# Kernel tuning notes

Measured on AMD Instinct MI355X. Metric: run time of the kernel, lower is better.

Reference implementation:

```python
import jax, jax.numpy as jnp
import numpy as np
from jax.scipy.special import logsumexp

SIGMA = 1.0
EPSILON = 1.0
MAX_ITER = 10


def _gaussian_kernel(x, y, sigma):
    # x: (b, l, d), y: (b, k, d) -> (b, l, k) negative-kernel matrix exp(-||x-y||^2 / (2 sigma^2))
    outer = jnp.einsum('bld,bkd->blk', x, y)
    norm_x = jnp.sum(x * x, axis=2)
    norm_y = jnp.sum(y * y, axis=2)
    dist = (norm_x[:, :, None] + norm_y[:, None, :] - 2.0 * outer) / (2.0 * sigma ** 2)
    return jnp.exp(-jnp.maximum(dist, 0.0))


def setup_inputs() -> dict:
    key = jax.random.key(0)
    kx, ka, ky, kb = jax.random.split(key, 4)
    B, L, K, D = 8, 2048, 2048, 32
    return {
        'x': jax.random.normal(kx, (B, L, D), dtype=jnp.float32),
        'a': jax.random.normal(ka, (B, L), dtype=jnp.float32),
        'y': jax.random.normal(ky, (B, K, D), dtype=jnp.float32),
        'b': jax.random.normal(kb, (B, K), dtype=jnp.float32),
    }


def _sinkhorn_potentials(x, a, y, b):
    sg = jax.lax.stop_gradient
    # Kernel matrices (carry gradient wrt x, y); weights a, b are detached inside kernels.
    Kxx = _gaussian_kernel(x, x, SIGMA) / EPSILON + sg(a)[:, None, :]
    Kyx_base = _gaussian_kernel(y, x, SIGMA)
    Kyx = Kyx_base / EPSILON + sg(a)[:, None, :]
    Kxy = jnp.swapaxes(Kyx_base, 1, 2) / EPSILON + sg(b)[:, None, :]
    Kyy = _gaussian_kernel(y, y, SIGMA) / EPSILON + sg(b)[:, None, :]

    # Sinkhorn loop runs under no_grad in the original: stop-gradient kernels.
    Kxx_s, Kyx_s, Kxy_s, Kyy_s = sg(Kxx), sg(Kyx), sg(Kxy), sg(Kyy)

    def step(carry, _):
        fxx, fyx, fxy, fyy = carry
        # sequential (Gauss-Seidel) update order matches the torch dict order xx, yx, xy, yy
        fxx = 0.5 * fxx - 0.5 * logsumexp(Kxx_s + fxx[:, None, :], axis=2)
        fyx = 0.5 * fyx - 0.5 * logsumexp(Kyx_s + fxy[:, None, :], axis=2)  # uses old fxy
        fxy = 0.5 * fxy - 0.5 * logsumexp(Kxy_s + fyx[:, None, :], axis=2)  # uses new fyx
        fyy = 0.5 * fyy - 0.5 * logsumexp(Kyy_s + fyy[:, None, :], axis=2)
        return (fxx, fyx, fxy, fyy), None

    init = (jnp.zeros_like(a), jnp.zeros_like(b), jnp.zeros_like(a), jnp.zeros_like(b))
    (fxx, fyx, fxy, fyy), _ = jax.lax.scan(step, init, None, length=MAX_ITER)

    # Final differentiable extrapolation step (potentials are detached constants).
    fe_xx = -logsumexp(Kxx + fxx[:, None, :], axis=2)
    fe_yx = -logsumexp(Kyx + fxy[:, None, :], axis=2)
    fe_xy = -logsumexp(Kxy + fyx[:, None, :], axis=2)
    fe_yy = -logsumexp(Kyy + fyy[:, None, :], axis=2)
    f = fe_xy - fe_xx  # (b, l)
    g = fe_yx - fe_yy  # (b, k)
    return f, g


def reference(x, a, y, b):
    f, g = _sinkhorn_potentials(x, a, y, b)
    res = jnp.sum(f * jnp.exp(a), axis=1) + jnp.sum(g * jnp.exp(b), axis=1)
    return res * EPSILON  # (batch,)
```

## Files before the change

kernel.cpp:

```cpp
#include <hip/hip_runtime.h>
#include <hip/hip_bf16.h>

#define B_ 8
#define N_ 2048
#define D_ 32
#define CAP 4096
#define EM1_DIAG 1.7182818284590452f

typedef __attribute__((ext_vector_type(8))) short short8;
typedef __attribute__((ext_vector_type(4))) float f32x4;

__global__ void setup_kernel(const float* __restrict__ x, const float* __restrict__ y,
                             unsigned short* __restrict__ xb, unsigned short* __restrict__ yb,
                             float* __restrict__ NX, float* __restrict__ NY,
                             int* __restrict__ cnt)
{
    int t = blockIdx.x * 256 + threadIdx.x;
    const float* src = (t < 16384) ? x : y;
    unsigned short* dstb = (t < 16384) ? xb : yb;
    float* dstn = (t < 16384) ? NX : NY;
    int row = (t < 16384) ? t : (t - 16384);
    const float* p = src + (size_t)row * D_;
    float ss = 0.f;
    unsigned short tmp[D_];
    #pragma unroll
    for (int k = 0; k < D_; k++) {
        float v = p[k];
        ss = fmaf(v, v, ss);
        __hip_bfloat16 h = __float2bfloat16(v);
        tmp[k] = *reinterpret_cast<unsigned short*>(&h);
    }
    #pragma unroll
    for (int k = 0; k < D_; k++) dstb[(size_t)row * D_ + k] = tmp[k];
    dstn[row] = ss * 0.5f;
    if (t < 24) cnt[t] = 0;
}

__global__ __launch_bounds__(256) void discover_kernel(
    const unsigned short* __restrict__ xb, const unsigned short* __restrict__ yb,
    const float* __restrict__ NX, const float* __restrict__ NY,
    int* __restrict__ cnt, uint2* __restrict__ lists)
{
    int m = blockIdx.x >> 8;
    int rem = blockIdx.x & 255;
    int batch = rem >> 5;
    int rowblk = rem & 31;
    const unsigned short* rd = (m == 0) ? xb : yb;
    const float*          rN = (m == 0) ? NX : NY;
    const unsigned short* cd = (m == 1) ? yb : xb;
    const float*          cN = (m == 1) ? NY : NX;

    const int tid = threadIdx.x, lane = tid & 63, wv = tid >> 6;
    const int r0 = rowblk * 64;
    const size_t rowbase = (size_t)batch * N_ + r0;

    short8 afrag[4];
    f32x4 cinit[4];
    #pragma unroll
    for (int g = 0; g < 4; g++) {
        afrag[g] = *reinterpret_cast<const short8*>(
            rd + (rowbase + g * 16 + (lane & 15)) * D_ + (lane >> 4) * 8);
        #pragma unroll
        for (int r = 0; r < 4; r++)
            cinit[g][r] = -rN[rowbase + g * 16 + (lane >> 4) * 4 + r];
    }
    const unsigned short* cdB = cd + (size_t)batch * N_ * D_;
    const float* cNB = cN + batch * N_;
    const int slot = m * 8 + batch;
    uint2* L = lists + (size_t)slot * CAP;

    #pragma unroll 4
    for (int cc = 0; cc < 32; ++cc) {
        int col = wv * 512 + cc * 16 + (lane & 15);
        short8 bfrag = *reinterpret_cast<const short8*>(
            cdB + (size_t)col * D_ + (lane >> 4) * 8);
        float ny = cNB[col];
        f32x4 d[4];
        #pragma unroll
        for (int g = 0; g < 4; g++)
            d[g] = __builtin_amdgcn_mfma_f32_16x16x32_bf16(afrag[g], bfrag, cinit[g], 0, 0, 0);
        float mx = d[0][0];
        #pragma unroll
        for (int g = 0; g < 4; g++)
            #pragma unroll
            for (int r = 0; r < 4; r++) mx = fmaxf(mx, d[g][r]);
        if (__any(mx > ny - 10.0f)) {
            #pragma unroll
            for (int g = 0; g < 4; g++) {
                #pragma unroll
                for (int r = 0; r < 4; r++) {
                    float dist = ny - d[g][r];
                    if (dist < 10.0f) {
                        int i = r0 + g * 16 + (lane >> 4) * 4 + r;
                        if (m == 2 || i != col) {
                            float Gv = __expf(-fmaxf(dist, 0.f));
                            float em1 = __expf(Gv) - 1.0f;
                            int idx = atomicAdd(&cnt[slot], 1);
                            if (idx < CAP)
                                L[idx] = make_uint2(((unsigned)i << 16) | (unsigned)col,
                                                    __float_as_uint(em1));
                        }
                    }
                }
            }
        }
    }
}

__global__ __launch_bounds__(1024) void sinkhorn_kernel(
    const float* __restrict__ a_in, const float* __restrict__ b_in,
    const int* __restrict__ cnt, const uint2* __restrict__ lists,
    float* __restrict__ out)
{
    __shared__ float f[4][N_];
    __shared__ float wsh[2][N_];
    __shared__ float ev[N_];
    __shared__ float acc[N_];
    __shared__ float red[16], red2[16];
    __shared__ float resacc;

    const int batch = blockIdx.x;
    const int t = threadIdx.x, lane = t & 63, wv = t >> 6;

    #pragma unroll
    for (int q = 0; q < 2; q++) {
        int j = t + 1024 * q;
        wsh[0][j] = a_in[batch * N_ + j];
        wsh[1][j] = b_in[batch * N_ + j];
        f[0][j] = 0.f; f[1][j] = 0.f; f[2][j] = 0.f; f[3][j] = 0.f;
    }
    if (t == 0) resacc = 0.f;

    const int nxx = min(cnt[0 * 8 + batch], CAP);
    const int nyy = min(cnt[1 * 8 + batch], CAP);
    const int nyx = min(cnt[2 * 8 + batch], CAP);
    const uint2* Lxx = lists + (size_t)(0 * 8 + batch) * CAP;
    const uint2* Lyy = lists + (size_t)(1 * 8 + batch) * CAP;
    const uint2* Lyx = lists + (size_t)(2 * 8 + batch) * CAP;
    __syncthreads();

    auto pass = [&](const float* wc, const float* cfv, float* fd,
                    const uint2* L, int n, bool tr, bool diag,
                    bool fin, const float* rw, float sgn) {
        float c0 = wc[t] + cfv[t];
        float c1 = wc[t + 1024] + cfv[t + 1024];
        float mloc = fmaxf(c0, c1);
        #pragma unroll
        for (int off = 1; off < 64; off <<= 1)
            mloc = fmaxf(mloc, __shfl_xor(mloc, off, 64));
        if (lane == 0) red[wv] = mloc;
        __syncthreads();
        float M = red[0];
        #pragma unroll
        for (int k = 1; k < 16; k++) M = fmaxf(M, red[k]);
        float e0 = __expf(c0 - M), e1 = __expf(c1 - M);
        ev[t] = e0; ev[t + 1024] = e1;
        acc[t]        = diag ? e0 * EM1_DIAG : 0.f;
        acc[t + 1024] = diag ? e1 * EM1_DIAG : 0.f;
        float ss = e0 + e1;
        #pragma unroll
        for (int off = 1; off < 64; off <<= 1)
            ss += __shfl_xor(ss, off, 64);
        if (lane == 0) red2[wv] = ss;
        __syncthreads();
        float S0 = red2[0];
        #pragma unroll
        for (int k = 1; k < 16; k++) S0 += red2[k];
        for (int p = t; p < n; p += 1024) {
            uint2 ent = L[p];
            int i = tr ? (int)(ent.x & 0xFFFFu) : (int)(ent.x >> 16);
            int j = tr ? (int)(ent.x >> 16)     : (int)(ent.x & 0xFFFFu);
            atomicAdd(&acc[i], ev[j] * __uint_as_float(ent.y));
        }
        __syncthreads();
        float r0v = M + __logf(S0 + acc[t]);
        float r1v = M + __logf(S0 + acc[t + 1024]);
        if (!fin) {
            fd[t]        = 0.5f * fd[t]        - 0.5f * r0v;
            fd[t + 1024] = 0.5f * fd[t + 1024] - 0.5f * r1v;
        } else {
            float ctr = sgn * (-r0v) * __expf(rw[t])
                      + sgn * (-r1v) * __expf(rw[t + 1024]);
            #pragma unroll
            for (int off = 1; off < 64; off <<= 1)
                ctr += __shfl_xor(ctr, off, 64);
            if (lane == 0) atomicAdd(&resacc, ctr);
        }
        __syncthreads();
    };

    for (int it = 0; it < 10; ++it) {
        pass(wsh[0], f[0], f[0], Lxx, nxx, false, true,  false, nullptr, 0.f);
        pass(wsh[0], f[2], f[1], Lyx, nyx, false, false, false, nullptr, 0.f);
        pass(wsh[1], f[1], f[2], Lyx, nyx, true,  false, false, nullptr, 0.f);
        pass(wsh[1], f[3], f[3], Lyy, nyy, false, true,  false, nullptr, 0.f);
    }
    pass(wsh[0], f[0], nullptr, Lxx, nxx, false, true,  true, wsh[0], -1.f);
    pass(wsh[0], f[2], nullptr, Lyx, nyx, false, false, true, wsh[1], +1.f);
    pass(wsh[1], f[1], nullptr, Lyx, nyx, true,  false, true, wsh[0], +1.f);
    pass(wsh[1], f[3], nullptr, Lyy, nyy, false, true,  true, wsh[1], -1.f);

    if (t == 0) out[batch] = resacc;
}

extern "C" void kernel_launch(void* const* d_in, const int* in_sizes, int n_in,
                              void* d_out, int out_size, void* d_ws, size_t ws_size,
                              hipStream_t stream)
{
    const float* x = (const float*)d_in[0];
    const float* a = (const float*)d_in[1];
    const float* y = (const float*)d_in[2];
    const float* b = (const float*)d_in[3];
    float* out = (float*)d_out;

    char* ws = (char*)d_ws;
    size_t o = 0;
    unsigned short* xb = (unsigned short*)(ws + o); o += (size_t)B_ * N_ * D_ * 2;
    unsigned short* yb = (unsigned short*)(ws + o); o += (size_t)B_ * N_ * D_ * 2;
    float* NX = (float*)(ws + o); o += (size_t)B_ * N_ * 4;
    float* NY = (float*)(ws + o); o += (size_t)B_ * N_ * 4;
    int* cnt = (int*)(ws + o); o += 128;
    uint2* lists = (uint2*)(ws + o); o += (size_t)3 * 8 * CAP * 8;

    setup_kernel<<<128, 256, 0, stream>>>(x, y, xb, yb, NX, NY, cnt);
    discover_kernel<<<3 * 256, 256, 0, stream>>>(xb, yb, NX, NY, cnt, lists);
    sinkhorn_kernel<<<B_, 1024, 0, stream>>>(a, b, cnt, lists, out);
}
```

Measured before the change: 205.9 us.

## Merge independent Sinkhorn passes per stage and use a fixed logsumexp shift

The xx, yx and yy potential updates do not depend on each other, so they now run together in one stage. The dependent xy update runs in a second stage, which removes about half of the block-wide barriers per iteration. The per-pass max reduction is replaced by a constant shift (M=8) with exp(a-8) and exp(b-8) computed once up front, and the first 2048 sparse-list entries are held in registers across iterations. The fixed shift assumes that weights and potentials stay within float exp range, which trades numerical robustness on extreme inputs for fewer reductions.

```diff
diff --git a/kernel.cpp b/kernel.cpp
--- a/kernel.cpp
+++ b/kernel.cpp
@@ -6,6 +6,8 @@
 #define D_ 32
 #define CAP 4096
 #define EM1_DIAG 1.7182818284590452f
+#define M_   8.0f
+#define EM_  2980.9579870417283f
 
 typedef __attribute__((ext_vector_type(8))) short short8;
 typedef __attribute__((ext_vector_type(4))) float f32x4;
@@ -113,23 +115,14 @@
     float* __restrict__ out)
 {
     __shared__ float f[4][N_];
-    __shared__ float wsh[2][N_];
-    __shared__ float ev[N_];
-    __shared__ float acc[N_];
-    __shared__ float red[16], red2[16];
+    __shared__ float ew[2][N_];
+    __shared__ float ev[4][N_];
+    __shared__ float acc[4][N_];
+    __shared__ float red2[4][16];
     __shared__ float resacc;
 
     const int batch = blockIdx.x;
     const int t = threadIdx.x, lane = t & 63, wv = t >> 6;
-
-    #pragma unroll
-    for (int q = 0; q < 2; q++) {
-        int j = t + 1024 * q;
-        wsh[0][j] = a_in[batch * N_ + j];
-        wsh[1][j] = b_in[batch * N_ + j];
-        f[0][j] = 0.f; f[1][j] = 0.f; f[2][j] = 0.f; f[3][j] = 0.f;
-    }
-    if (t == 0) resacc = 0.f;
 
     const int nxx = min(cnt[0 * 8 + batch], CAP);
     const int nyy = min(cnt[1 * 8 + batch], CAP);
@@ -137,70 +130,149 @@
     const uint2* Lxx = lists + (size_t)(0 * 8 + batch) * CAP;
     const uint2* Lyy = lists + (size_t)(1 * 8 + batch) * CAP;
     const uint2* Lyx = lists + (size_t)(2 * 8 + batch) * CAP;
+
+    uint2 rxx[2], ryy[2], ryx[2];
+    #pragma unroll
+    for (int q = 0; q < 2; q++) {
+        int p = t + 1024 * q;
+        rxx[q] = (p < nxx) ? Lxx[p] : make_uint2(0u, 0u);
+        ryy[q] = (p < nyy) ? Lyy[p] : make_uint2(0u, 0u);
+        ryx[q] = (p < nyx) ? Lyx[p] : make_uint2(0u, 0u);
+    }
+
+    #pragma unroll
+    for (int q = 0; q < 2; q++) {
+        int j = t + 1024 * q;
+        ew[0][j] = __expf(a_in[batch * N_ + j] - M_);
+        ew[1][j] = __expf(b_in[batch * N_ + j] - M_);
+        f[0][j] = 0.f; f[1][j] = 0.f; f[2][j] = 0.f; f[3][j] = 0.f;
+    }
+    if (t == 0) resacc = 0.f;
     __syncthreads();
 
-    auto pass = [&](const float* wc, const float* cfv, float* fd,
-                    const uint2* L, int n, bool tr, bool diag,
-                    bool fin, const float* rw, float sgn) {
-        float c0 = wc[t] + cfv[t];
-        float c1 = wc[t + 1024] + cfv[t + 1024];
-        float mloc = fmaxf(c0, c1);
-        #pragma unroll
-        for (int off = 1; off < 64; off <<= 1)
-            mloc = fmaxf(mloc, __shfl_xor(mloc, off, 64));
-        if (lane == 0) red[wv] = mloc;
-        __syncthreads();
-        float M = red[0];
-        #pragma unroll
-        for (int k = 1; k < 16; k++) M = fmaxf(M, red[k]);
-        float e0 = __expf(c0 - M), e1 = __expf(c1 - M);
-        ev[t] = e0; ev[t + 1024] = e1;
-        acc[t]        = diag ? e0 * EM1_DIAG : 0.f;
-        acc[t + 1024] = diag ? e1 * EM1_DIAG : 0.f;
-        float ss = e0 + e1;
-        #pragma unroll
-        for (int off = 1; off < 64; off <<= 1)
-            ss += __shfl_xor(ss, off, 64);
-        if (lane == 0) red2[wv] = ss;
-        __syncthreads();
-        float S0 = red2[0];
-        #pragma unroll
-        for (int k = 1; k < 16; k++) S0 += red2[k];
-        for (int p = t; p < n; p += 1024) {
-            uint2 ent = L[p];
-            int i = tr ? (int)(ent.x & 0xFFFFu) : (int)(ent.x >> 16);
-            int j = tr ? (int)(ent.x >> 16)     : (int)(ent.x & 0xFFFFu);
-            atomicAdd(&acc[i], ev[j] * __uint_as_float(ent.y));
-        }
-        __syncthreads();
-        float r0v = M + __logf(S0 + acc[t]);
-        float r1v = M + __logf(S0 + acc[t + 1024]);
-        if (!fin) {
-            fd[t]        = 0.5f * fd[t]        - 0.5f * r0v;
-            fd[t + 1024] = 0.5f * fd[t + 1024] - 0.5f * r1v;
-        } else {
-            float ctr = sgn * (-r0v) * __expf(rw[t])
-                      + sgn * (-r1v) * __expf(rw[t + 1024]);
-            #pragma unroll
-            for (int off = 1; off < 64; off <<= 1)
-                ctr += __shfl_xor(ctr, off, 64);
-            if (lane == 0) atomicAdd(&resacc, ctr);
+    auto stageA = [&]() {
+        float ss0 = 0.f, ss1 = 0.f, ss2 = 0.f;
+        #pragma unroll
+        for (int q = 0; q < 2; q++) {
+            int j = t + 1024 * q;
+            float e0 = ew[0][j] * __expf(f[0][j]); ev[0][j] = e0; acc[0][j] = e0 * EM1_DIAG; ss0 += e0;
+            float e1 = ew[0][j] * __expf(f[2][j]); ev[1][j] = e1; acc[1][j] = 0.f;           ss1 += e1;
+            float e2 = ew[1][j] * __expf(f[3][j]); ev[2][j] = e2; acc[2][j] = e2 * EM1_DIAG; ss2 += e2;
+        }
+        #pragma unroll
+        for (int off = 1; off < 64; off <<= 1) {
+            ss0 += __shfl_xor(ss0, off, 64);
+            ss1 += __shfl_xor(ss1, off, 64);
+            ss2 += __shfl_xor(ss2, off, 64);
+        }
+        if (lane == 0) { red2[0][wv] = ss0; red2[1][wv] = ss1; red2[2][wv] = ss2; }
+        __syncthreads();
+        float S0 = red2[0][0], S1 = red2[1][0], S2 = red2[2][0];
+        #pragma unroll
+        for (int k = 1; k < 16; k++) { S0 += red2[0][k]; S1 += red2[1][k]; S2 += red2[2][k]; }
+        #pragma unroll
+        for (int q = 0; q < 2; q++) {
+            int p = t + 1024 * q;
+            if (p < nxx) { uint2 e = rxx[q]; atomicAdd(&acc[0][e.x >> 16], ev[0][e.x & 0xFFFFu] * __uint_as_float(e.y)); }
+            if (p < nyx) { uint2 e = ryx[q]; atomicAdd(&acc[1][e.x >> 16], ev[1][e.x & 0xFFFFu] * __uint_as_float(e.y)); }
+            if (p < nyy) { uint2 e = ryy[q]; atomicAdd(&acc[2][e.x >> 16], ev[2][e.x & 0xFFFFu] * __uint_as_float(e.y)); }
+        }
+        for (int p = 2048 + t; p < nxx; p += 1024) { uint2 e = Lxx[p]; atomicAdd(&acc[0][e.x >> 16], ev[0][e.x & 0xFFFFu] * __uint_as_float(e.y)); }
+        for (int p = 2048 + t; p < nyx; p += 1024) { uint2 e = Lyx[p]; atomicAdd(&acc[1][e.x >> 16], ev[1][e.x & 0xFFFFu] * __uint_as_float(e.y)); }
+        for (int p = 2048 + t; p < nyy; p += 1024) { uint2 e = Lyy[p]; atomicAdd(&acc[2][e.x >> 16], ev[2][e.x & 0xFFFFu] * __uint_as_float(e.y)); }
+        __syncthreads();
+        #pragma unroll
+        for (int q = 0; q < 2; q++) {
+            int i = t + 1024 * q;
+            f[0][i] = 0.5f * f[0][i] - 0.5f * (M_ + __logf(S0 + acc[0][i]));
+            f[1][i] = 0.5f * f[1][i] - 0.5f * (M_ + __logf(S1 + acc[1][i]));
+            f[3][i] = 0.5f * f[3][i] - 0.5f * (M_ + __logf(S2 + acc[2][i]));
         }
         __syncthreads();
     };
 
-    for (int it = 0; it < 10; ++it) {
-        pass(wsh[0], f[0], f[0], Lxx, nxx, false, true,  false, nullptr, 0.f);
-        pass(wsh[0], f[2], f[1], Lyx, nyx, false, false, false, nullptr, 0.f);
-        pass(wsh[1], f[1], f[2], Lyx, nyx, true,  false, false, nullptr, 0.f);
-        pass(wsh[1], f[3], f[3], Lyy, nyy, false, true,  false, nullptr, 0.f);
-    }
-    pass(wsh[0], f[0], nullptr, Lxx, nxx, false, true,  true, wsh[0], -1.f);
-    pass(wsh[0], f[2], nullptr, Lyx, nyx, false, false, true, wsh[1], +1.f);
-    pass(wsh[1], f[1], nullptr, Lyx, nyx, true,  false, true, wsh[0], +1.f);
-    pass(wsh[1], f[3], nullptr, Lyy, nyy, false, true,  true, wsh[1], -1.f);
-
-    if (t == 0) out[batch] = resacc;
+    auto stageB = [&]() {
+        float ss0 = 0.f;
+        #pragma unroll
+        for (int q = 0; q < 2; q++) {
+            int j = t + 1024 * q;
+            float e0 = ew[1][j] * __expf(f[1][j]); ev[0][j] = e0; acc[0][j] = 0.f; ss0 += e0;
+        }
+        #pragma unroll
+        for (int off = 1; off < 64; off <<= 1) ss0 += __shfl_xor(ss0, off, 64);
+        if (lane == 0) red2[0][wv] = ss0;
+        __syncthreads();
+        float S0 = red2[0][0];
+        #pragma unroll
+        for (int k = 1; k < 16; k++) S0 += red2[0][k];
+        #pragma unroll
+        for (int q = 0; q < 2; q++) {
+            int p = t + 1024 * q;
+            if (p < nyx) { uint2 e = ryx[q]; atomicAdd(&acc[0][e.x & 0xFFFFu], ev[0][e.x >> 16] * __uint_as_float(e.y)); }
+        }
+        for (int p = 2048 + t; p < nyx; p += 1024) { uint2 e = Lyx[p]; atomicAdd(&acc[0][e.x & 0xFFFFu], ev[0][e.x >> 16] * __uint_as_float(e.y)); }
+        __syncthreads();
+        #pragma unroll
+        for (int q = 0; q < 2; q++) {
+            int i = t + 1024 * q;
+            f[2][i] = 0.5f * f[2][i] - 0.5f * (M_ + __logf(S0 + acc[0][i]));
+        }
+        __syncthreads();
+    };
+
+    for (int it = 0; it < 10; ++it) { stageA(); stageB(); }
+
+    {
+        float ss0 = 0.f, ss1 = 0.f, ss2 = 0.f, ss3 = 0.f;
+        #pragma unroll
+        for (int q = 0; q < 2; q++) {
+            int j = t + 1024 * q;
+            float e0 = ew[0][j] * __expf(f[0][j]); ev[0][j] = e0; acc[0][j] = e0 * EM1_DIAG; ss0 += e0;
+            float e1 = ew[0][j] * __expf(f[2][j]); ev[1][j] = e1; acc[1][j] = 0.f;           ss1 += e1;
+            float e2 = ew[1][j] * __expf(f[1][j]); ev[2][j] = e2; acc[2][j] = 0.f;           ss2 += e2;
+            float e3 = ew[1][j] * __expf(f[3][j]); ev[3][j] = e3; acc[3][j] = e3 * EM1_DIAG; ss3 += e3;
+        }
+        #pragma unroll
+        for (int off = 1; off < 64; off <<= 1) {
+            ss0 += __shfl_xor(ss0, off, 64);
+            ss1 += __shfl_xor(ss1, off, 64);
+            ss2 += __shfl_xor(ss2, off, 64);
+            ss3 += __shfl_xor(ss3, off, 64);
+        }
+        if (lane == 0) { red2[0][wv] = ss0; red2[1][wv] = ss1; red2[2][wv] = ss2; red2[3][wv] = ss3; }
+        __syncthreads();
+        float S0 = red2[0][0], S1 = red2[1][0], S2 = red2[2][0], S3 = red2[3][0];
+        #pragma unroll
+        for (int k = 1; k < 16; k++) { S0 += red2[0][k]; S1 += red2[1][k]; S2 += red2[2][k]; S3 += red2[3][k]; }
+        #pragma unroll
+        for (int q = 0; q < 2; q++) {
+            int p = t + 1024 * q;
+            if (p < nxx) { uint2 e = rxx[q]; atomicAdd(&acc[0][e.x >> 16],    ev[0][e.x & 0xFFFFu] * __uint_as_float(e.y)); }
+            if (p < nyx) { uint2 e = ryx[q]; atomicAdd(&acc[1][e.x >> 16],    ev[1][e.x & 0xFFFFu] * __uint_as_float(e.y));
+                                             atomicAdd(&acc[2][e.x & 0xFFFFu], ev[2][e.x >> 16]    * __uint_as_float(e.y)); }
+            if (p < nyy) { uint2 e = ryy[q]; atomicAdd(&acc[3][e.x >> 16],    ev[3][e.x & 0xFFFFu] * __uint_as_float(e.y)); }
+        }
+        for (int p = 2048 + t; p < nxx; p += 1024) { uint2 e = Lxx[p]; atomicAdd(&acc[0][e.x >> 16], ev[0][e.x & 0xFFFFu] * __uint_as_float(e.y)); }
+        for (int p = 2048 + t; p < nyx; p += 1024) { uint2 e = Lyx[p]; atomicAdd(&acc[1][e.x >> 16], ev[1][e.x & 0xFFFFu] * __uint_as_float(e.y));
+                                                     atomicAdd(&acc[2][e.x & 0xFFFFu], ev[2][e.x >> 16] * __uint_as_float(e.y)); }
+        for (int p = 2048 + t; p < nyy; p += 1024) { uint2 e = Lyy[p]; atomicAdd(&acc[3][e.x >> 16], ev[3][e.x & 0xFFFFu] * __uint_as_float(e.y)); }
+        __syncthreads();
+        float ctr = 0.f;
+        #pragma unroll
+        for (int q = 0; q < 2; q++) {
+            int i = t + 1024 * q;
+            float r0 = M_ + __logf(S0 + acc[0][i]);
+            float r1 = M_ + __logf(S1 + acc[1][i]);
+            float r2 = M_ + __logf(S2 + acc[2][i]);
+            float r3 = M_ + __logf(S3 + acc[3][i]);
+            ctr += (r0 - r2) * ew[0][i] * EM_ + (r3 - r1) * ew[1][i] * EM_;
+        }
+        #pragma unroll
+        for (int off = 1; off < 64; off <<= 1) ctr += __shfl_xor(ctr, off, 64);
+        if (lane == 0) atomicAdd(&resacc, ctr);
+        __syncthreads();
+        if (t == 0) out[batch] = resacc;
+    }
 }
 
 extern "C" void kernel_launch(void* const* d_in, const int* in_sizes, int n_in,
```

Measured after the change: 178.9 us. 1.15x faster.

## Switch sparse correction lists to per-row CSR and fuse independent Sinkhorn passes

Applied to the files above, without the earlier changes.

Sparse near-neighbour corrections are now stored in fixed-capacity per-row buckets instead of one global atomic list per matrix. The Sinkhorn loop can then gather per row rather than scatter with shared-memory atomics. The per-pass max reduction is replaced by a fixed shift M, since a and f are bounded, and the independent xx, yx and yy updates are fused into one stage with double-buffered exp vectors, removing many barriers. Discovery is split into a mask pass and a recompute pass. The risks are overflow of the 16-entry row cap, a fixed-shift exp that could under- or overflow for other inputs, and a larger workspace.

```diff
diff --git a/kernel.cpp b/kernel.cpp
--- a/kernel.cpp
+++ b/kernel.cpp
@@ -4,8 +4,10 @@
 #define B_ 8
 #define N_ 2048
 #define D_ 32
-#define CAP 4096
+#define RCAP 16
 #define EM1_DIAG 1.7182818284590452f
+#define M_   8.0f
+#define EM_  2980.9579870417283f
 
 typedef __attribute__((ext_vector_type(8))) short short8;
 typedef __attribute__((ext_vector_type(4))) float f32x4;
@@ -13,33 +15,43 @@
 __global__ void setup_kernel(const float* __restrict__ x, const float* __restrict__ y,
                              unsigned short* __restrict__ xb, unsigned short* __restrict__ yb,
                              float* __restrict__ NX, float* __restrict__ NY,
-                             int* __restrict__ cnt)
+                             int* __restrict__ csr_cnt)
 {
     int t = blockIdx.x * 256 + threadIdx.x;
     const float* src = (t < 16384) ? x : y;
     unsigned short* dstb = (t < 16384) ? xb : yb;
     float* dstn = (t < 16384) ? NX : NY;
     int row = (t < 16384) ? t : (t - 16384);
-    const float* p = src + (size_t)row * D_;
+    const float4* p = reinterpret_cast<const float4*>(src + (size_t)row * D_);
     float ss = 0.f;
-    unsigned short tmp[D_];
-    #pragma unroll
-    for (int k = 0; k < D_; k++) {
-        float v = p[k];
-        ss = fmaf(v, v, ss);
-        __hip_bfloat16 h = __float2bfloat16(v);
-        tmp[k] = *reinterpret_cast<unsigned short*>(&h);
-    }
-    #pragma unroll
-    for (int k = 0; k < D_; k++) dstb[(size_t)row * D_ + k] = tmp[k];
+    float4 v[8];
+    #pragma unroll
+    for (int k = 0; k < 8; k++) {
+        v[k] = p[k];
+        ss += v[k].x * v[k].x + v[k].y * v[k].y + v[k].z * v[k].z + v[k].w * v[k].w;
+    }
+    short8* dst8 = reinterpret_cast<short8*>(dstb + (size_t)row * D_);
+    #pragma unroll
+    for (int k = 0; k < 4; k++) {
+        const float fv[8] = { v[2*k].x, v[2*k].y, v[2*k].z, v[2*k].w,
+                              v[2*k+1].x, v[2*k+1].y, v[2*k+1].z, v[2*k+1].w };
+        short8 o;
+        #pragma unroll
+        for (int e = 0; e < 8; e++) {
+            __hip_bfloat16 h = __float2bfloat16(fv[e]);
+            o[e] = *reinterpret_cast<const short*>(&h);
+        }
+        dst8[k] = o;
+    }
     dstn[row] = ss * 0.5f;
-    if (t < 24) cnt[t] = 0;
+    csr_cnt[2 * t] = 0;
+    csr_cnt[2 * t + 1] = 0;
 }
 
 __global__ __launch_bounds__(256) void discover_kernel(
     const unsigned short* __restrict__ xb, const unsigned short* __restrict__ yb,
     const float* __restrict__ NX, const float* __restrict__ NY,
-    int* __restrict__ cnt, uint2* __restrict__ lists)
+    int* __restrict__ csr_cnt, uint2* __restrict__ csr_ent)
 {
     int m = blockIdx.x >> 8;
     int rem = blockIdx.x & 255;
@@ -60,18 +72,18 @@
     for (int g = 0; g < 4; g++) {
         afrag[g] = *reinterpret_cast<const short8*>(
             rd + (rowbase + g * 16 + (lane & 15)) * D_ + (lane >> 4) * 8);
-        #pragma unroll
-        for (int r = 0; r < 4; r++)
-            cinit[g][r] = -rN[rowbase + g * 16 + (lane >> 4) * 4 + r];
+        float4 nv = *reinterpret_cast<const float4*>(
+            rN + rowbase + g * 16 + (lane >> 4) * 4);
+        cinit[g][0] = -nv.x; cinit[g][1] = -nv.y; cinit[g][2] = -nv.z; cinit[g][3] = -nv.w;
     }
     const unsigned short* cdB = cd + (size_t)batch * N_ * D_;
     const float* cNB = cN + batch * N_;
-    const int slot = m * 8 + batch;
-    uint2* L = lists + (size_t)slot * CAP;
-
-    #pragma unroll 4
+    const int c0w = wv * 512;
+
+    unsigned mask = 0;
+    #pragma unroll 8
     for (int cc = 0; cc < 32; ++cc) {
-        int col = wv * 512 + cc * 16 + (lane & 15);
+        int col = c0w + cc * 16 + (lane & 15);
         short8 bfrag = *reinterpret_cast<const short8*>(
             cdB + (size_t)col * D_ + (lane >> 4) * 8);
         float ny = cNB[col];
@@ -79,27 +91,45 @@
         #pragma unroll
         for (int g = 0; g < 4; g++)
             d[g] = __builtin_amdgcn_mfma_f32_16x16x32_bf16(afrag[g], bfrag, cinit[g], 0, 0, 0);
-        float mx = d[0][0];
+        float m0 = fmaxf(fmaxf(d[0][0], d[0][1]), fmaxf(d[0][2], d[0][3]));
+        float m1 = fmaxf(fmaxf(d[1][0], d[1][1]), fmaxf(d[1][2], d[1][3]));
+        float m2 = fmaxf(fmaxf(d[2][0], d[2][1]), fmaxf(d[2][2], d[2][3]));
+        float m3 = fmaxf(fmaxf(d[3][0], d[3][1]), fmaxf(d[3][2], d[3][3]));
+        float mx = fmaxf(fmaxf(m0, m1), fmaxf(m2, m3));
+        mask |= (__any(mx > ny - 10.0f) ? 1u : 0u) << cc;
+    }
+
+    auto push = [&](int T, int row, int colv, float em1) {
+        size_t base = (size_t)(T * B_ + batch) * N_ + row;
+        int idx = atomicAdd(&csr_cnt[base], 1);
+        if (idx < RCAP)
+            csr_ent[base * RCAP + idx] = make_uint2((unsigned)colv, __float_as_uint(em1));
+    };
+    while (mask) {
+        int cc = __builtin_ctz(mask);
+        mask &= mask - 1;
+        int col = c0w + cc * 16 + (lane & 15);
+        short8 bfrag = *reinterpret_cast<const short8*>(
+            cdB + (size_t)col * D_ + (lane >> 4) * 8);
+        float ny = cNB[col];
+        f32x4 d[4];
         #pragma unroll
         for (int g = 0; g < 4; g++)
+            d[g] = __builtin_amdgcn_mfma_f32_16x16x32_bf16(afrag[g], bfrag, cinit[g], 0, 0, 0);
+        #pragma unroll
+        for (int g = 0; g < 4; g++) {
             #pragma unroll
-            for (int r = 0; r < 4; r++) mx = fmaxf(mx, d[g][r]);
-        if (__any(mx > ny - 10.0f)) {
-            #pragma unroll
-            for (int g = 0; g < 4; g++) {
-                #pragma unroll
-                for (int r = 0; r < 4; r++) {
-                    float dist = ny - d[g][r];
-                    if (dist < 10.0f) {
-                        int i = r0 + g * 16 + (lane >> 4) * 4 + r;
-                        if (m == 2 || i != col) {
-                            float Gv = __expf(-fmaxf(dist, 0.f));
-                            float em1 = __expf(Gv) - 1.0f;
-                            int idx = atomicAdd(&cnt[slot], 1);
-                            if (idx < CAP)
-                                L[idx] = make_uint2(((unsigned)i << 16) | (unsigned)col,
-                                                    __float_as_uint(em1));
-                        }
+            for (int r = 0; r < 4; r++) {
+                float dist = ny - d[g][r];
+                if (dist < 10.0f) {
+                    int i = r0 + g * 16 + (lane >> 4) * 4 + r;
+                    if (m == 2) {
+                        float em1 = __expf(__expf(-fmaxf(dist, 0.f))) - 1.0f;
+                        push(2, i, col, em1);
+                        push(3, col, i, em1);
+                    } else if (i != col) {
+                        float em1 = __expf(__expf(-fmaxf(dist, 0.f))) - 1.0f;
+                        push(m, i, col, em1);
                     }
                 }
             }
@@ -107,100 +137,145 @@
     }
 }
 
-__global__ __launch_bounds__(1024) void sinkhorn_kernel(
+__device__ __forceinline__ float tree8(const float* r) {
+    return ((r[0] + r[1]) + (r[2] + r[3])) + ((r[4] + r[5]) + (r[6] + r[7]));
+}
+
+__global__ __launch_bounds__(512) void sinkhorn_kernel(
     const float* __restrict__ a_in, const float* __restrict__ b_in,
-    const int* __restrict__ cnt, const uint2* __restrict__ lists,
+    const int* __restrict__ csr_cnt, const uint2* __restrict__ csr_ent,
     float* __restrict__ out)
 {
     __shared__ float f[4][N_];
-    __shared__ float wsh[2][N_];
-    __shared__ float ev[N_];
-    __shared__ float acc[N_];
-    __shared__ float red[16], red2[16];
+    __shared__ float ew[2][N_];
+    __shared__ float evb[2][4][N_];
+    __shared__ float red2[2][4][8];
     __shared__ float resacc;
 
     const int batch = blockIdx.x;
     const int t = threadIdx.x, lane = t & 63, wv = t >> 6;
 
-    #pragma unroll
-    for (int q = 0; q < 2; q++) {
-        int j = t + 1024 * q;
-        wsh[0][j] = a_in[batch * N_ + j];
-        wsh[1][j] = b_in[batch * N_ + j];
+    int cnts[4][4];
+    const uint2* ebase[4];
+    #pragma unroll
+    for (int T = 0; T < 4; T++) {
+        size_t bb = (size_t)(T * B_ + batch) * N_;
+        ebase[T] = csr_ent + bb * RCAP;
+        #pragma unroll
+        for (int q = 0; q < 4; q++)
+            cnts[T][q] = min(csr_cnt[bb + t + 512 * q], RCAP);
+    }
+    #pragma unroll
+    for (int q = 0; q < 4; q++) {
+        int j = t + 512 * q;
+        ew[0][j] = __expf(a_in[batch * N_ + j] - M_);
+        ew[1][j] = __expf(b_in[batch * N_ + j] - M_);
         f[0][j] = 0.f; f[1][j] = 0.f; f[2][j] = 0.f; f[3][j] = 0.f;
     }
     if (t == 0) resacc = 0.f;
 
-    const int nxx = min(cnt[0 * 8 + batch], CAP);
-    const int nyy = min(cnt[1 * 8 + batch], CAP);
-    const int nyx = min(cnt[2 * 8 + batch], CAP);
-    const uint2* Lxx = lists + (size_t)(0 * 8 + batch) * CAP;
-    const uint2* Lyy = lists + (size_t)(1 * 8 + batch) * CAP;
-    const uint2* Lyx = lists + (size_t)(2 * 8 + batch) * CAP;
-    __syncthreads();
-
-    auto pass = [&](const float* wc, const float* cfv, float* fd,
-                    const uint2* L, int n, bool tr, bool diag,
-                    bool fin, const float* rw, float sgn) {
-        float c0 = wc[t] + cfv[t];
-        float c1 = wc[t + 1024] + cfv[t + 1024];
-        float mloc = fmaxf(c0, c1);
-        #pragma unroll
-        for (int off = 1; off < 64; off <<= 1)
-            mloc = fmaxf(mloc, __shfl_xor(mloc, off, 64));
-        if (lane == 0) red[wv] = mloc;
+    auto gath = [&](const uint2* E, int cnt, const float* evbuf) -> float {
+        float g = 0.f;
+        for (int k = 0; k < cnt; ++k) {
+            uint2 e = E[k];
+            g += evbuf[e.x] * __uint_as_float(e.y);
+        }
+        return g;
+    };
+    auto wred = [&](float& s) {
+        #pragma unroll
+        for (int off = 1; off < 64; off <<= 1) s += __shfl_xor(s, off, 64);
+    };
+
+    auto stageA = [&](int par) {
+        float s0 = 0.f, s1 = 0.f, s2 = 0.f;
+        float e0q[4], e2q[4], f0o[4], f1o[4], f3o[4];
+        #pragma unroll
+        for (int q = 0; q < 4; q++) {
+            int j = t + 512 * q;
+            f0o[q] = f[0][j]; f1o[q] = f[1][j]; float f2v = f[2][j]; f3o[q] = f[3][j];
+            float e0 = ew[0][j] * __expf(f0o[q]); evb[par][0][j] = e0; e0q[q] = e0; s0 += e0;
+            float e1 = ew[0][j] * __expf(f2v);    evb[par][1][j] = e1;              s1 += e1;
+            float e2 = ew[1][j] * __expf(f3o[q]); evb[par][2][j] = e2; e2q[q] = e2; s2 += e2;
+        }
+        wred(s0); wred(s1); wred(s2);
+        if (lane == 0) { red2[par][0][wv] = s0; red2[par][1][wv] = s1; red2[par][2][wv] = s2; }
         __syncthreads();
-        float M = red[0];
-        #pragma unroll
-        for (int k = 1; k < 16; k++) M = fmaxf(M, red[k]);
-        float e0 = __expf(c0 - M), e1 = __expf(c1 - M);
-        ev[t] = e0; ev[t + 1024] = e1;
-        acc[t]        = diag ? e0 * EM1_DIAG : 0.f;
-        acc[t + 1024] = diag ? e1 * EM1_DIAG : 0.f;
-        float ss = e0 + e1;
-        #pragma unroll
-        for (int off = 1; off < 64; off <<= 1)
-            ss += __shfl_xor(ss, off, 64);
-        if (lane == 0) red2[wv] = ss;
+        float S0 = tree8(red2[par][0]), S1 = tree8(red2[par][1]), S2 = tree8(red2[par][2]);
+        #pragma unroll
+        for (int q = 0; q < 4; q++) {
+            int i = t + 512 * q;
+            float g0 = gath(ebase[0] + (size_t)i * RCAP, cnts[0][q], evb[par][0]);
+            f[0][i] = 0.5f * f0o[q] - 0.5f * (M_ + __logf(S0 + e0q[q] * EM1_DIAG + g0));
+            float g1 = gath(ebase[2] + (size_t)i * RCAP, cnts[2][q], evb[par][1]);
+            f[1][i] = 0.5f * f1o[q] - 0.5f * (M_ + __logf(S1 + g1));
+            float g2 = gath(ebase[1] + (size_t)i * RCAP, cnts[1][q], evb[par][2]);
+            f[3][i] = 0.5f * f3o[q] - 0.5f * (M_ + __logf(S2 + e2q[q] * EM1_DIAG + g2));
+        }
+    };
+
+    auto stageB = [&](int par) {
+        float sB = 0.f;
+        float f2o[4];
+        #pragma unroll
+        for (int q = 0; q < 4; q++) {
+            int j = t + 512 * q;
+            f2o[q] = f[2][j];
+            float ee = ew[1][j] * __expf(f[1][j]); evb[par][0][j] = ee; sB += ee;
+        }
+        wred(sB);
+        if (lane == 0) red2[par][0][wv] = sB;
         __syncthreads();
-        float S0 = red2[0];
-        #pragma unroll
-        for (int k = 1; k < 16; k++) S0 += red2[k];
-        for (int p = t; p < n; p += 1024) {
-            uint2 ent = L[p];
-            int i = tr ? (int)(ent.x & 0xFFFFu) : (int)(ent.x >> 16);
-            int j = tr ? (int)(ent.x >> 16)     : (int)(ent.x & 0xFFFFu);
-            atomicAdd(&acc[i], ev[j] * __uint_as_float(ent.y));
-        }
+        float S = tree8(red2[par][0]);
+        #pragma unroll
+        for (int q = 0; q < 4; q++) {
+            int i = t + 512 * q;
+            float g = gath(ebase[3] + (size_t)i * RCAP, cnts[3][q], evb[par][0]);
+            f[2][i] = 0.5f * f2o[q] - 0.5f * (M_ + __logf(S + g));
+        }
+    };
+
+    int s = 0;
+    for (int it = 0; it < 10; ++it) {
+        stageA(s & 1); s++;
+        stageB(s & 1); s++;
+    }
+
+    {
+        int par = s & 1;
+        float s0 = 0.f, s1 = 0.f, s2 = 0.f, s3 = 0.f;
+        float e0q[4], e3q[4];
+        #pragma unroll
+        for (int q = 0; q < 4; q++) {
+            int j = t + 512 * q;
+            float e0 = ew[0][j] * __expf(f[0][j]); evb[par][0][j] = e0; e0q[q] = e0; s0 += e0;
+            float e1 = ew[0][j] * __expf(f[2][j]); evb[par][1][j] = e1;              s1 += e1;
+            float e2 = ew[1][j] * __expf(f[1][j]); evb[par][2][j] = e2;              s2 += e2;
+            float e3 = ew[1][j] * __expf(f[3][j]); evb[par][3][j] = e3; e3q[q] = e3; s3 += e3;
+        }
+        wred(s0); wred(s1); wred(s2); wred(s3);
+        if (lane == 0) { red2[par][0][wv] = s0; red2[par][1][wv] = s1;
+                         red2[par][2][wv] = s2; red2[par][3][wv] = s3; }
         __syncthreads();
-        float r0v = M + __logf(S0 + acc[t]);
-        float r1v = M + __logf(S0 + acc[t + 1024]);
-        if (!fin) {
-            fd[t]        = 0.5f * fd[t]        - 0.5f * r0v;
-            fd[t + 1024] = 0.5f * fd[t + 1024] - 0.5f * r1v;
-        } else {
-            float ctr = sgn * (-r0v) * __expf(rw[t])
-                      + sgn * (-r1v) * __expf(rw[t + 1024]);
-            #pragma unroll
-            for (int off = 1; off < 64; off <<= 1)
-                ctr += __shfl_xor(ctr, off, 64);
-            if (lane == 0) atomicAdd(&resacc, ctr);
-        }
+        float S0 = tree8(red2[par][0]), S1 = tree8(red2[par][1]);
+        float S2 = tree8(red2[par][2]), S3 = tree8(red2[par][3]);
+        float ctr = 0.f;
+        #pragma unroll
+        for (int q = 0; q < 4; q++) {
+            int i = t + 512 * q;
+            float r0 = M_ + __logf(S0 + e0q[q] * EM1_DIAG +
+                                   gath(ebase[0] + (size_t)i * RCAP, cnts[0][q], evb[par][0]));
+            float r1 = M_ + __logf(S1 + gath(ebase[2] + (size_t)i * RCAP, cnts[2][q], evb[par][1]));
+            float r2 = M_ + __logf(S2 + gath(ebase[3] + (size_t)i * RCAP, cnts[3][q], evb[par][2]));
+            float r3 = M_ + __logf(S3 + e3q[q] * EM1_DIAG +
+                                   gath(ebase[1] + (size_t)i * RCAP, cnts[1][q], evb[par][3]));
+            ctr += (r0 - r2) * ew[0][i] * EM_ + (r3 - r1) * ew[1][i] * EM_;
+        }
+        wred(ctr);
+        if (lane == 0) atomicAdd(&resacc, ctr);
         __syncthreads();
-    };
-
-    for (int it = 0; it < 10; ++it) {
-        pass(wsh[0], f[0], f[0], Lxx, nxx, false, true,  false, nullptr, 0.f);
-        pass(wsh[0], f[2], f[1], Lyx, nyx, false, false, false, nullptr, 0.f);
-        pass(wsh[1], f[1], f[2], Lyx, nyx, true,  false, false, nullptr, 0.f);
-        pass(wsh[1], f[3], f[3], Lyy, nyy, false, true,  false, nullptr, 0.f);
-    }
-    pass(wsh[0], f[0], nullptr, Lxx, nxx, false, true,  true, wsh[0], -1.f);
-    pass(wsh[0], f[2], nullptr, Lyx, nyx, false, false, true, wsh[1], +1.f);
-    pass(wsh[1], f[1], nullptr, Lyx, nyx, true,  false, true, wsh[0], +1.f);
-    pass(wsh[1], f[3], nullptr, Lyy, nyy, false, true,  true, wsh[1], -1.f);
-
-    if (t == 0) out[batch] = resacc;
+        if (t == 0) out[batch] = resacc;
+    }
 }
 
 extern "C" void kernel_launch(void* const* d_in, const int* in_sizes, int n_in,
@@ -219,10 +294,10 @@
     unsigned short* yb = (unsigned short*)(ws + o); o += (size_t)B_ * N_ * D_ * 2;
     float* NX = (float*)(ws + o); o += (size_t)B_ * N_ * 4;
     float* NY = (float*)(ws + o); o += (size_t)B_ * N_ * 4;
-    int* cnt = (int*)(ws + o); o += 128;
-    uint2* lists = (uint2*)(ws + o); o += (size_t)3 * 8 * CAP * 8;
-
-    setup_kernel<<<128, 256, 0, stream>>>(x, y, xb, yb, NX, NY, cnt);
-    discover_kernel<<<3 * 256, 256, 0, stream>>>(xb, yb, NX, NY, cnt, lists);
-    sinkhorn_kernel<<<B_, 1024, 0, stream>>>(a, b, cnt, lists, out);
-}
+    int* csr_cnt = (int*)(ws + o); o += (size_t)4 * B_ * N_ * 4;
+    uint2* csr_ent = (uint2*)(ws + o); o += (size_t)4 * B_ * N_ * RCAP * 8;
+
+    setup_kernel<<<128, 256, 0, stream>>>(x, y, xb, yb, NX, NY, csr_cnt);
+    discover_kernel<<<3 * 256, 256, 0, stream>>>(xb, yb, NX, NY, csr_cnt, csr_ent);
+    sinkhorn_kernel<<<B_, 512, 0, stream>>>(a, b, csr_cnt, csr_ent, out);
+}
```

Measured after the change: 207.7 us. No clear change (+0.9%).
